# Kernel optimization log

Measured on AMD Instinct MI355X. Metric: run time of the kernel, lower is better.

The kernel has to match this reference:

```python
import jax, jax.numpy as jnp
import numpy as np

# Cost coefficients from MatcherConfig (init_kwargs)
C_CLASS, C_MASK, C_DICE, C_DIST, C_NLL, C_LIK = 2.0, 5.0, 5.0, 1.0, 0.5, 0.5

B, P, Q, E = 8, 16384, 256, 128  # images, pixels (H*W), queries, electrons


def setup_inputs() -> dict:
    key = jax.random.key(0)
    ks = jax.random.split(key, 8)
    mask_mask = jax.random.uniform(ks[0], (B, P, Q)) < 0.10           # sparsity pattern of pred logits
    mask_logit_values = jax.random.normal(ks[1], (B, P, Q), jnp.float32)
    seg_occ = jax.random.uniform(ks[2], (B, P, E)) < 0.05              # sparsity pattern of target segmap
    seg_vals = jax.random.uniform(ks[3], (B, P, E), jnp.float32, 1e-3, 1.0)
    segmap_values = jnp.where(seg_occ, seg_vals, 0.0)
    pred_logits = jax.random.normal(ks[4], (B, Q), jnp.float32)
    pred_positions = jax.random.uniform(ks[5], (B, Q, 2), jnp.float32)
    true_positions = jax.random.uniform(ks[6], (B, E, 2), jnp.float32)
    kd, ko = jax.random.split(ks[7])
    diag = 1.0 + 2.0 * jax.random.uniform(kd, (B, Q, 2), jnp.float32)  # positive diag of scale_tril
    off = 0.3 * jax.random.normal(ko, (B, Q), jnp.float32)
    pred_chol = jnp.zeros((B, Q, 2, 2), jnp.float32)
    pred_chol = pred_chol.at[..., 0, 0].set(diag[..., 0])
    pred_chol = pred_chol.at[..., 1, 1].set(diag[..., 1])
    pred_chol = pred_chol.at[..., 1, 0].set(off)
    image_sizes_xy = jnp.full((B, 2), 128.0, jnp.float32)
    return {
        'pred_logits': pred_logits,
        'mask_logit_values': mask_logit_values,
        'mask_mask': mask_mask,
        'segmap_values': segmap_values,
        'pred_positions': pred_positions,
        'pred_chol': pred_chol,
        'true_positions': true_positions,
        'image_sizes_xy': image_sizes_xy,
    }


def _total_cost(pred_logits, mask_logit_values, segmap_values, pred_positions,
                pred_chol, true_positions, image_sizes_xy, mask_mask):
    sp = jax.nn.softplus
    m = mask_mask
    # --- class cost: BCE(logit, 1) per query -> [B,Q]
    class_cost = sp(-pred_logits)
    # --- mask BCE cost (get_bce_cost): sparse entries only
    pos = jnp.where(m, sp(-mask_logit_values), 0.0)   # BCE vs 1 on nnz entries
    neg = jnp.where(m, sp(mask_logit_values), 0.0)    # BCE vs 0 on nnz entries
    targ = (segmap_values > 0).astype(pos.dtype)      # binarized target segmap
    pos_loss = jnp.einsum('bpq,bpe->bqe', pos, targ)
    neg_loss = neg.sum(1)[:, :, None] - jnp.einsum('bpq,bpe->bqe', neg, targ)
    nnz = jnp.maximum(targ.sum((1, 2)), 1.0)          # target _nnz() per image
    mask_cost = (pos_loss + neg_loss) / nnz[:, None, None]
    # --- dice cost (get_dice_cost): sparse softmax over query dim
    NEG = jnp.asarray(-1e30, mask_logit_values.dtype)
    z = jnp.where(m, mask_logit_values, NEG)
    mx = jnp.max(z, axis=-1, keepdims=True)
    ez = jnp.where(m, jnp.exp(z - mx), 0.0)
    s = ez.sum(-1, keepdims=True)
    pred_p = jnp.where(s > 0, ez / jnp.maximum(s, 1e-30), 0.0)  # [B,P,Q]
    num = 2.0 * jnp.einsum('bpq,bpe->bqe', pred_p, segmap_values)
    den = pred_p.sum(1)[:, :, None] + segmap_values.sum(1)[:, None, :]
    dice_cost = 1.0 - (num + 1.0) / (den + 1.0)
    # --- huber distance cost (delta=1), mean over xy
    d = pred_positions[:, :, None, :] - true_positions[:, None, :, :]  # [B,Q,E,2]
    ad = jnp.abs(d)
    huber_cost = jnp.where(ad < 1.0, 0.5 * d * d, ad - 0.5).mean(-1)
    # --- NLL / likelihood distance costs (MVN with scale_tril)
    mu = pred_positions * image_sizes_xy[:, None, :]
    y = true_positions * image_sizes_xy[:, None, :]
    diff = y[:, None, :, :] - mu[:, :, None, :]        # [B,Q,E,2]
    L00 = pred_chol[..., 0, 0][:, :, None]
    L10 = pred_chol[..., 1, 0][:, :, None]
    L11 = pred_chol[..., 1, 1][:, :, None]
    z0 = diff[..., 0] / L00
    z1 = (diff[..., 1] - L10 * z0) / L11
    nll_cost = 0.5 * (z0 * z0 + z1 * z1) + jnp.log(2.0 * jnp.pi) + jnp.log(L00) + jnp.log(L11)
    lik_cost = 1.0 - jnp.exp(-nll_cost)
    total = (C_CLASS * class_cost[:, :, None] + C_MASK * mask_cost + C_DICE * dice_cost
             + C_DIST * huber_cost + C_NLL * nll_cost + C_LIK * lik_cost)
    return total  # [B, Q, E] stacked per-image cost matrices


def reference(pred_logits, mask_logit_values, mask_mask, segmap_values,
              pred_positions, pred_chol, true_positions, image_sizes_xy):
    return _total_cost(pred_logits, mask_logit_values, segmap_values, pred_positions,
                       pred_chol, true_positions, image_sizes_xy, mask_mask)
```

## Files before the change

kernel.cpp:

```cpp
#include <hip/hip_runtime.h>
#include <cstdint>
#include <cstddef>

typedef float v4f __attribute__((ext_vector_type(4)));
typedef short short8 __attribute__((ext_vector_type(8)));

constexpr int B_ = 8, P_ = 16384, Q_ = 256, E_ = 128;

__device__ __forceinline__ unsigned int f2bf(float f) {
  unsigned int x = __float_as_uint(f);
  x += 0x7FFFu + ((x >> 16) & 1u);
  return x >> 16;
}
__device__ __forceinline__ float softplus_f(float x) {
  return fmaxf(x, 0.f) + __logf(1.f + __expf(-fabsf(x)));
}
__device__ __forceinline__ float wsum(float v) {
#pragma unroll
  for (int o = 32; o; o >>= 1) v += __shfl_xor(v, o, 64);
  return v;
}
__device__ __forceinline__ void lds_barrier() {
  asm volatile("s_waitcnt lgkmcnt(0)" ::: "memory");
  __builtin_amdgcn_s_barrier();
}

#define ZW 15360
__device__ __forceinline__ short8 ldfrag(const unsigned int* lds, int rowbase, int quad) {
  const int a = (quad < 2) ? (rowbase + 4 * quad) : ZW;
  union { unsigned int u[4]; short8 s; } x;
  *(uint2*)(x.u)     = *(const uint2*)(lds + a);
  *(uint2*)(x.u + 2) = *(const uint2*)(lds + a + 2);
  return x.s;
}

template<bool DIRECT>
__global__ __launch_bounds__(1024) void fused_all(
    const float* __restrict__ mlv, const int* __restrict__ mask,
    const float* __restrict__ seg, float* __restrict__ part,
    float* __restrict__ negsum, float* __restrict__ ppsum,
    float* __restrict__ segsum, float* __restrict__ nnzb)
{
  __shared__ __align__(16) unsigned int lds[15376];

  const int t = threadIdx.x, w = t >> 6, l = t & 63;
  const int lm = l & 15, quad = l >> 4;
  const int wr = w & 3, wc = w >> 2;
  const int kw = w >> 1, kh = w & 1;
  const int b = blockIdx.x >> 5, ks = blockIdx.x & 31;

  if (t < 4) lds[ZW + t] = 0u;

  v4f acc0[4][2], acc1[4][2];
#pragma unroll
  for (int i = 0; i < 4; ++i)
#pragma unroll
    for (int j = 0; j < 2; ++j) { acc0[i][j] = (v4f)0.f; acc1[i][j] = (v4f)0.f; }
  float accN[4] = {0.f,0.f,0.f,0.f};
  float accP[4] = {0.f,0.f,0.f,0.f};
  float accS[2] = {0.f,0.f};
  float cnt = 0.f;

  const float* mp = mlv + ((size_t)b * P_ + ks * 512 + w) * Q_ + l;
  const int*   kp = mask + ((size_t)b * P_ + ks * 512 + w) * Q_ + l;
  const float* sp = seg + ((size_t)b * P_ + ks * 512 + w) * E_ + l;

  float X[4]; int M[4]; float S[2];
#pragma unroll
  for (int j = 0; j < 4; ++j) { X[j] = mp[64 * j]; M[j] = kp[64 * j]; }
  S[0] = sp[0]; S[1] = sp[64];

  for (int it = 0; it < 32; ++it) {
    const int bb = (it & 1) * 7680;

    float xs[4]; int ms[4]; float sv[2];
#pragma unroll
    for (int j = 0; j < 4; ++j) { xs[j] = X[j]; ms[j] = M[j]; }
    sv[0] = S[0]; sv[1] = S[1];

    if (it < 31) {
      mp += 16 * Q_; kp += 16 * Q_; sp += 16 * E_;
#pragma unroll
      for (int j = 0; j < 4; ++j) { X[j] = mp[64 * j]; M[j] = kp[64 * j]; }
      S[0] = sp[0]; S[1] = sp[64];
    }

    float ez[4], s = 0.f;
#pragma unroll
    for (int j = 0; j < 4; ++j) {
      const float e = ms[j] ? __expf(xs[j]) : 0.f;
      ez[j] = e; s += e;
      accN[j] += __logf(1.f + e);
    }
    s = wsum(s);
    const float inv = (s > 0.f) ? (1.f / s) : 0.f;

    unsigned short* hs = (unsigned short*)lds;
#pragma unroll
    for (int j = 0; j < 4; ++j) {
      const int q = l + 64 * j;
      const float p = ez[j] * inv;
      accP[j] += p;
      hs[(bb + q * 10 + kw) * 2 + kh]        = (unsigned short)f2bf(ms[j] ? -xs[j] : 0.f);
      hs[(bb + 2560 + q * 10 + kw) * 2 + kh] = (unsigned short)f2bf(p);
    }
#pragma unroll
    for (int jj = 0; jj < 2; ++jj) {
      const int e = l + 64 * jj;
      accS[jj] += sv[jj];
      cnt += (sv[jj] > 0.f) ? 1.f : 0.f;
      hs[(bb + 5120 + e * 10 + kw) * 2 + kh] = (sv[jj] > 0.f) ? (unsigned short)0x3F80 : (unsigned short)0;
      hs[(bb + 6400 + e * 10 + kw) * 2 + kh] = (unsigned short)f2bf(sv[jj]);
    }

    lds_barrier();

#pragma unroll
    for (int j2 = 0; j2 < 2; ++j2) {
      const int eb = wc * 32 + j2 * 16 + lm;
      const short8 bf0 = ldfrag(lds, bb + 5120 + eb * 10, quad);
      const short8 bf1 = ldfrag(lds, bb + 6400 + eb * 10, quad);
#pragma unroll
      for (int i = 0; i < 4; ++i) {
        const int qa = wr * 64 + i * 16 + lm;
        const short8 af0 = ldfrag(lds, bb + qa * 10, quad);
        const short8 af1 = ldfrag(lds, bb + 2560 + qa * 10, quad);
        acc0[i][j2] = __builtin_amdgcn_mfma_f32_16x16x32_bf16(af0, bf0, acc0[i][j2], 0, 0, 0);
        acc1[i][j2] = __builtin_amdgcn_mfma_f32_16x16x32_bf16(af1, bf1, acc1[i][j2], 0, 0, 0);
      }
    }
  }

  __syncthreads();
  float* fr = (float*)lds;
#pragma unroll
  for (int j = 0; j < 4; ++j) {
    fr[w * 256 + l + 64 * j] = accN[j];
    fr[4096 + w * 256 + l + 64 * j] = accP[j];
  }
#pragma unroll
  for (int jj = 0; jj < 2; ++jj)
    fr[8192 + w * 128 + l + 64 * jj] = accS[jj];
  __syncthreads();
  if (t < 256) {
    float sn = 0.f, sq = 0.f;
#pragma unroll
    for (int k = 0; k < 16; ++k) { sn += fr[k * 256 + t]; sq += fr[4096 + k * 256 + t]; }
    atomicAdd(&negsum[b * 256 + t], sn);
    atomicAdd(&ppsum[b * 256 + t], sq);
  } else if (t < 384) {
    const int e = t - 256;
    float ss = 0.f;
#pragma unroll
    for (int k = 0; k < 16; ++k) ss += fr[8192 + k * 128 + e];
    atomicAdd(&segsum[b * 128 + e], ss);
  }
  cnt = wsum(cnt);
  if (l == 0) atomicAdd(&nnzb[b], cnt);

  if constexpr (DIRECT) {
    float* p0 = part + ((size_t)(ks * 8 + b) * 2) * 32768;
    float* p1 = p0 + 32768;
#pragma unroll
    for (int i = 0; i < 4; ++i)
#pragma unroll
      for (int r = 0; r < 4; ++r) {
        const int q = wr * 64 + i * 16 + quad * 4 + r;
#pragma unroll
        for (int j2 = 0; j2 < 2; ++j2) {
          const int e = wc * 32 + j2 * 16 + lm;
          p0[q * 128 + e] = acc0[i][j2][r];
          p1[q * 128 + e] = acc1[i][j2][r];
        }
      }
  } else {
    float* p0 = part + (size_t)b * 32768;
    float* p1 = part + (size_t)(8 + b) * 32768;
#pragma unroll
    for (int i = 0; i < 4; ++i)
#pragma unroll
      for (int r = 0; r < 4; ++r) {
        const int q = wr * 64 + i * 16 + quad * 4 + r;
#pragma unroll
        for (int j2 = 0; j2 < 2; ++j2) {
          const int e = wc * 32 + j2 * 16 + lm;
          atomicAdd(&p0[q * 128 + e], acc0[i][j2][r]);
          atomicAdd(&p1[q * 128 + e], acc1[i][j2][r]);
        }
      }
  }
}

template<bool DIRECT>
__global__ __launch_bounds__(128) void epilogue(
    const float* __restrict__ part,
    const float* __restrict__ negsum, const float* __restrict__ ppsum,
    const float* __restrict__ segsum, const float* __restrict__ nnzb,
    const float* __restrict__ logits, const float* __restrict__ ppos,
    const float* __restrict__ chol, const float* __restrict__ tpos,
    const float* __restrict__ imgsz, float* __restrict__ out)
{
  const int bq = blockIdx.x;
  const int b = bq >> 8;
  const int e = threadIdx.x;
  const int qe = (bq & 255) * 128 + e;

  float g1, g2;
  if constexpr (DIRECT) {
    g1 = 0.f; g2 = 0.f;
#pragma unroll 8
    for (int ksi = 0; ksi < 32; ++ksi) {
      g1 += part[((size_t)(ksi * 8 + b) * 2) * 32768 + qe];
      g2 += part[((size_t)(ksi * 8 + b) * 2 + 1) * 32768 + qe];
    }
  } else {
    g1 = part[(size_t)b * 32768 + qe];
    g2 = part[(size_t)(8 + b) * 32768 + qe];
  }

  const float nnz = fmaxf(nnzb[b], 1.f);
  const float mask_cost = (negsum[bq] + g1) / nnz;
  const float dice = 1.f - (2.f * g2 + 1.f) / (ppsum[bq] + segsum[b * 128 + e] + 1.f);
  const float cls = softplus_f(-logits[bq]);
  const float px = ppos[bq * 2], py = ppos[bq * 2 + 1];
  const float tx = tpos[(b * 128 + e) * 2], ty = tpos[(b * 128 + e) * 2 + 1];
  const float dx = px - tx, dy = py - ty;
  const float ax = fabsf(dx), ay = fabsf(dy);
  const float hx = (ax < 1.f) ? 0.5f * dx * dx : ax - 0.5f;
  const float hy = (ay < 1.f) ? 0.5f * dy * dy : ay - 0.5f;
  const float huber = 0.5f * (hx + hy);
  const float sx = imgsz[b * 2], sy = imgsz[b * 2 + 1];
  const float L00 = chol[bq * 4 + 0], L10 = chol[bq * 4 + 2], L11 = chol[bq * 4 + 3];
  const float d0 = (tx - px) * sx, d1 = (ty - py) * sy;
  const float z0 = d0 / L00;
  const float z1 = (d1 - L10 * z0) / L11;
  const float nll = 0.5f * (z0 * z0 + z1 * z1) + 1.8378770664093453f + __logf(L00) + __logf(L11);
  const float lik = 1.f - __expf(-nll);
  out[bq * 128 + e] = 2.f * cls + 5.f * mask_cost + 5.f * dice + huber + 0.5f * nll + 0.5f * lik;
}

extern "C" void kernel_launch(void* const* d_in, const int* in_sizes, int n_in,
                              void* d_out, int out_size, void* d_ws, size_t ws_size,
                              hipStream_t stream)
{
  (void)in_sizes; (void)n_in; (void)out_size;
  const float* logits = (const float*)d_in[0];
  const float* mlv    = (const float*)d_in[1];
  const int*   mask   = (const int*)d_in[2];
  const float* seg    = (const float*)d_in[3];
  const float* ppos   = (const float*)d_in[4];
  const float* chol   = (const float*)d_in[5];
  const float* tpos   = (const float*)d_in[6];
  const float* imgsz  = (const float*)d_in[7];

  char* ws = (char*)d_ws;
  const size_t PART_DIRECT = 67108864ull;
  const size_t NEED = PART_DIRECT + 20512ull;

  if (ws_size >= NEED) {
    float* part   = (float*)ws;
    float* negsum = (float*)(ws + PART_DIRECT);
    float* ppsum  = (float*)(ws + PART_DIRECT + 8192);
    float* segsum = (float*)(ws + PART_DIRECT + 16384);
    float* nnzb   = (float*)(ws + PART_DIRECT + 20480);
    hipMemsetAsync(ws + PART_DIRECT, 0, 20512, stream);
    fused_all<true><<<256, 1024, 0, stream>>>(mlv, mask, seg, part, negsum, ppsum, segsum, nnzb);
    epilogue<true><<<2048, 128, 0, stream>>>(part, negsum, ppsum, segsum, nnzb,
                                             logits, ppos, chol, tpos, imgsz, (float*)d_out);
  } else {
    float* part   = (float*)(ws);
    float* negsum = (float*)(ws + 2097152);
    float* ppsum  = (float*)(ws + 2105344);
    float* segsum = (float*)(ws + 2113536);
    float* nnzb   = (float*)(ws + 2117632);
    hipMemsetAsync(ws, 0, 2117664, stream);
    fused_all<false><<<256, 1024, 0, stream>>>(mlv, mask, seg, part, negsum, ppsum, segsum, nnzb);
    epilogue<false><<<2048, 128, 0, stream>>>(part, negsum, ppsum, segsum, nnzb,
                                              logits, ppos, chol, tpos, imgsz, (float*)d_out);
  }
}
```

Measured before the change: 457.0 us.

## Split expert dimension across blocks and repack LDS tiles as swizzled bf16 pairs

The fused kernel now launches 512 blocks of 512 threads, where each block covers half of the E columns. Each wave processes two pixels per step and writes packed 32-bit bf16 pairs into a single XOR-swizzled LDS buffer, so fragments can be read with 128-bit loads instead of scattered 16-bit stores and 64-bit reads. The aim is to cut LDS store and bank-conflict overhead and to raise occupancy with smaller blocks. In exchange, the mask logits, mask and exp/log work on the Q side are now read and computed twice, once per E half, and a second barrier replaces the double buffering.

```diff
diff --git a/kernel.cpp b/kernel.cpp
--- a/kernel.cpp
+++ b/kernel.cpp
@@ -25,31 +25,28 @@
   __builtin_amdgcn_s_barrier();
 }
 
-#define ZW 15360
-__device__ __forceinline__ short8 ldfrag(const unsigned int* lds, int rowbase, int quad) {
-  const int a = (quad < 2) ? (rowbase + 4 * quad) : ZW;
-  union { unsigned int u[4]; short8 s; } x;
-  *(uint2*)(x.u)     = *(const uint2*)(lds + a);
-  *(uint2*)(x.u + 2) = *(const uint2*)(lds + a + 2);
-  return x.s;
-}
-
 template<bool DIRECT>
-__global__ __launch_bounds__(1024) void fused_all(
+__global__ __launch_bounds__(512, 4) void fused_all(
     const float* __restrict__ mlv, const int* __restrict__ mask,
     const float* __restrict__ seg, float* __restrict__ part,
     float* __restrict__ negsum, float* __restrict__ ppsum,
     float* __restrict__ segsum, float* __restrict__ nnzb)
 {
-  __shared__ __align__(16) unsigned int lds[15376];
+  __shared__ __align__(16) unsigned int lds[5120];
+  unsigned int* A1 = lds;
+  unsigned int* EZ = lds + 2048;
+  unsigned int* SB = lds + 4096;
+  unsigned int* ST = lds + 4608;
 
   const int t = threadIdx.x, w = t >> 6, l = t & 63;
   const int lm = l & 15, quad = l >> 4;
   const int wr = w & 3, wc = w >> 2;
-  const int kw = w >> 1, kh = w & 1;
-  const int b = blockIdx.x >> 5, ks = blockIdx.x & 31;
-
-  if (t < 4) lds[ZW + t] = 0u;
+  const int eh = blockIdx.x >> 8;
+  const int b  = (blockIdx.x >> 5) & 7;
+  const int ks = blockIdx.x & 31;
+  const int wx   = w ^ ((l & 1) << 2);
+  const int qsel = 4 * (quad ^ (lm & 1));
+  const bool hasd = (quad < 2);
 
   v4f acc0[4][2], acc1[4][2];
 #pragma unroll
@@ -58,75 +55,85 @@
     for (int j = 0; j < 2; ++j) { acc0[i][j] = (v4f)0.f; acc1[i][j] = (v4f)0.f; }
   float accN[4] = {0.f,0.f,0.f,0.f};
   float accP[4] = {0.f,0.f,0.f,0.f};
-  float accS[2] = {0.f,0.f};
-  float cnt = 0.f;
-
-  const float* mp = mlv + ((size_t)b * P_ + ks * 512 + w) * Q_ + l;
-  const int*   kp = mask + ((size_t)b * P_ + ks * 512 + w) * Q_ + l;
-  const float* sp = seg + ((size_t)b * P_ + ks * 512 + w) * E_ + l;
-
-  float X[4]; int M[4]; float S[2];
-#pragma unroll
-  for (int j = 0; j < 4; ++j) { X[j] = mp[64 * j]; M[j] = kp[64 * j]; }
-  S[0] = sp[0]; S[1] = sp[64];
+  float accS = 0.f, cnt = 0.f;
+
+  const float* mp = mlv + ((size_t)b * P_ + ks * 512 + 2 * w) * Q_ + l;
+  const int*   kp = mask + ((size_t)b * P_ + ks * 512 + 2 * w) * Q_ + l;
+  const float* sp = seg + ((size_t)b * P_ + ks * 512 + 2 * w) * E_ + eh * 64 + l;
+
+  float X0[4], X1[4]; int M0[4], M1[4]; float S0, S1;
+#pragma unroll
+  for (int j = 0; j < 4; ++j) {
+    X0[j] = mp[64 * j]; X1[j] = mp[Q_ + 64 * j];
+    M0[j] = kp[64 * j]; M1[j] = kp[Q_ + 64 * j];
+  }
+  S0 = sp[0]; S1 = sp[E_];
 
   for (int it = 0; it < 32; ++it) {
-    const int bb = (it & 1) * 7680;
-
-    float xs[4]; int ms[4]; float sv[2];
-#pragma unroll
-    for (int j = 0; j < 4; ++j) { xs[j] = X[j]; ms[j] = M[j]; }
-    sv[0] = S[0]; sv[1] = S[1];
+    float ez0[4], ez1[4]; unsigned a1w[4];
+    float s0 = 0.f, s1 = 0.f;
+#pragma unroll
+    for (int j = 0; j < 4; ++j) {
+      const bool m0 = M0[j] != 0, m1 = M1[j] != 0;
+      a1w[j] = f2bf(m0 ? -X0[j] : 0.f) | (f2bf(m1 ? -X1[j] : 0.f) << 16);
+      const float e0 = m0 ? __expf(X0[j]) : 0.f;
+      const float e1 = m1 ? __expf(X1[j]) : 0.f;
+      ez0[j] = e0; ez1[j] = e1; s0 += e0; s1 += e1;
+      accN[j] += __logf(1.f + e0) + __logf(1.f + e1);
+    }
+    const unsigned sbw = ((S0 > 0.f) ? 0x3F80u : 0u) | ((S1 > 0.f) ? 0x3F800000u : 0u);
+    const unsigned stw = f2bf(S0) | (f2bf(S1) << 16);
+    accS += S0 + S1;
+    cnt  += ((S0 > 0.f) ? 1.f : 0.f) + ((S1 > 0.f) ? 1.f : 0.f);
 
     if (it < 31) {
       mp += 16 * Q_; kp += 16 * Q_; sp += 16 * E_;
 #pragma unroll
-      for (int j = 0; j < 4; ++j) { X[j] = mp[64 * j]; M[j] = kp[64 * j]; }
-      S[0] = sp[0]; S[1] = sp[64];
-    }
-
-    float ez[4], s = 0.f;
+      for (int j = 0; j < 4; ++j) {
+        X0[j] = mp[64 * j]; X1[j] = mp[Q_ + 64 * j];
+        M0[j] = kp[64 * j]; M1[j] = kp[Q_ + 64 * j];
+      }
+      S0 = sp[0]; S1 = sp[E_];
+    }
+
+    s0 = wsum(s0); s1 = wsum(s1);
+    const float i0 = (s0 > 0.f) ? (1.f / s0) : 0.f;
+    const float i1 = (s1 > 0.f) ? (1.f / s1) : 0.f;
+    unsigned ezw[4];
 #pragma unroll
     for (int j = 0; j < 4; ++j) {
-      const float e = ms[j] ? __expf(xs[j]) : 0.f;
-      ez[j] = e; s += e;
-      accN[j] += __logf(1.f + e);
-    }
-    s = wsum(s);
-    const float inv = (s > 0.f) ? (1.f / s) : 0.f;
-
-    unsigned short* hs = (unsigned short*)lds;
+      const float p0 = ez0[j] * i0, p1 = ez1[j] * i1;
+      accP[j] += p0 + p1;
+      ezw[j] = f2bf(p0) | (f2bf(p1) << 16);
+    }
+
+    lds_barrier();
 #pragma unroll
     for (int j = 0; j < 4; ++j) {
-      const int q = l + 64 * j;
-      const float p = ez[j] * inv;
-      accP[j] += p;
-      hs[(bb + q * 10 + kw) * 2 + kh]        = (unsigned short)f2bf(ms[j] ? -xs[j] : 0.f);
-      hs[(bb + 2560 + q * 10 + kw) * 2 + kh] = (unsigned short)f2bf(p);
-    }
-#pragma unroll
-    for (int jj = 0; jj < 2; ++jj) {
-      const int e = l + 64 * jj;
-      accS[jj] += sv[jj];
-      cnt += (sv[jj] > 0.f) ? 1.f : 0.f;
-      hs[(bb + 5120 + e * 10 + kw) * 2 + kh] = (sv[jj] > 0.f) ? (unsigned short)0x3F80 : (unsigned short)0;
-      hs[(bb + 6400 + e * 10 + kw) * 2 + kh] = (unsigned short)f2bf(sv[jj]);
-    }
-
+      A1[8 * l + 512 * j + wx] = a1w[j];
+      EZ[8 * l + 512 * j + wx] = ezw[j];
+    }
+    SB[8 * l + wx] = sbw;
+    ST[8 * l + wx] = stw;
     lds_barrier();
 
+    const short8 z8 = {0,0,0,0,0,0,0,0};
+    short8 af0[4], af1[4];
+#pragma unroll
+    for (int i = 0; i < 4; ++i) {
+      const int a = (wr * 64 + i * 16 + lm) * 8 + qsel;
+      af0[i] = hasd ? *(const short8*)(A1 + a) : z8;
+      af1[i] = hasd ? *(const short8*)(EZ + a) : z8;
+    }
 #pragma unroll
     for (int j2 = 0; j2 < 2; ++j2) {
-      const int eb = wc * 32 + j2 * 16 + lm;
-      const short8 bf0 = ldfrag(lds, bb + 5120 + eb * 10, quad);
-      const short8 bf1 = ldfrag(lds, bb + 6400 + eb * 10, quad);
+      const int bb = (wc * 32 + j2 * 16 + lm) * 8 + qsel;
+      const short8 bf0 = hasd ? *(const short8*)(SB + bb) : z8;
+      const short8 bf1 = hasd ? *(const short8*)(ST + bb) : z8;
 #pragma unroll
       for (int i = 0; i < 4; ++i) {
-        const int qa = wr * 64 + i * 16 + lm;
-        const short8 af0 = ldfrag(lds, bb + qa * 10, quad);
-        const short8 af1 = ldfrag(lds, bb + 2560 + qa * 10, quad);
-        acc0[i][j2] = __builtin_amdgcn_mfma_f32_16x16x32_bf16(af0, bf0, acc0[i][j2], 0, 0, 0);
-        acc1[i][j2] = __builtin_amdgcn_mfma_f32_16x16x32_bf16(af1, bf1, acc1[i][j2], 0, 0, 0);
+        acc0[i][j2] = __builtin_amdgcn_mfma_f32_16x16x32_bf16(af0[i], bf0, acc0[i][j2], 0, 0, 0);
+        acc1[i][j2] = __builtin_amdgcn_mfma_f32_16x16x32_bf16(af1[i], bf1, acc1[i][j2], 0, 0, 0);
       }
     }
   }
@@ -136,24 +143,24 @@
 #pragma unroll
   for (int j = 0; j < 4; ++j) {
     fr[w * 256 + l + 64 * j] = accN[j];
-    fr[4096 + w * 256 + l + 64 * j] = accP[j];
-  }
-#pragma unroll
-  for (int jj = 0; jj < 2; ++jj)
-    fr[8192 + w * 128 + l + 64 * jj] = accS[jj];
+    fr[2048 + w * 256 + l + 64 * j] = accP[j];
+  }
+  fr[4096 + w * 64 + l] = accS;
   __syncthreads();
   if (t < 256) {
     float sn = 0.f, sq = 0.f;
 #pragma unroll
-    for (int k = 0; k < 16; ++k) { sn += fr[k * 256 + t]; sq += fr[4096 + k * 256 + t]; }
-    atomicAdd(&negsum[b * 256 + t], sn);
-    atomicAdd(&ppsum[b * 256 + t], sq);
-  } else if (t < 384) {
+    for (int k = 0; k < 8; ++k) { sn += fr[k * 256 + t]; sq += fr[2048 + k * 256 + t]; }
+    if (eh == 0) {
+      atomicAdd(&negsum[b * 256 + t], sn);
+      atomicAdd(&ppsum[b * 256 + t], sq);
+    }
+  } else if (t < 320) {
     const int e = t - 256;
     float ss = 0.f;
 #pragma unroll
-    for (int k = 0; k < 16; ++k) ss += fr[8192 + k * 128 + e];
-    atomicAdd(&segsum[b * 128 + e], ss);
+    for (int k = 0; k < 8; ++k) ss += fr[4096 + k * 64 + e];
+    atomicAdd(&segsum[b * 128 + eh * 64 + e], ss);
   }
   cnt = wsum(cnt);
   if (l == 0) atomicAdd(&nnzb[b], cnt);
@@ -168,9 +175,9 @@
         const int q = wr * 64 + i * 16 + quad * 4 + r;
 #pragma unroll
         for (int j2 = 0; j2 < 2; ++j2) {
-          const int e = wc * 32 + j2 * 16 + lm;
-          p0[q * 128 + e] = acc0[i][j2][r];
-          p1[q * 128 + e] = acc1[i][j2][r];
+          const int eg = eh * 64 + wc * 32 + j2 * 16 + lm;
+          p0[q * 128 + eg] = acc0[i][j2][r];
+          p1[q * 128 + eg] = acc1[i][j2][r];
         }
       }
   } else {
@@ -183,9 +190,9 @@
         const int q = wr * 64 + i * 16 + quad * 4 + r;
 #pragma unroll
         for (int j2 = 0; j2 < 2; ++j2) {
-          const int e = wc * 32 + j2 * 16 + lm;
-          atomicAdd(&p0[q * 128 + e], acc0[i][j2][r]);
-          atomicAdd(&p1[q * 128 + e], acc1[i][j2][r]);
+          const int eg = eh * 64 + wc * 32 + j2 * 16 + lm;
+          atomicAdd(&p0[q * 128 + eg], acc0[i][j2][r]);
+          atomicAdd(&p1[q * 128 + eg], acc1[i][j2][r]);
         }
       }
   }
@@ -264,7 +271,7 @@
     float* segsum = (float*)(ws + PART_DIRECT + 16384);
     float* nnzb   = (float*)(ws + PART_DIRECT + 20480);
     hipMemsetAsync(ws + PART_DIRECT, 0, 20512, stream);
-    fused_all<true><<<256, 1024, 0, stream>>>(mlv, mask, seg, part, negsum, ppsum, segsum, nnzb);
+    fused_all<true><<<512, 512, 0, stream>>>(mlv, mask, seg, part, negsum, ppsum, segsum, nnzb);
     epilogue<true><<<2048, 128, 0, stream>>>(part, negsum, ppsum, segsum, nnzb,
                                              logits, ppos, chol, tpos, imgsz, (float*)d_out);
   } else {
@@ -274,7 +281,7 @@
     float* segsum = (float*)(ws + 2113536);
     float* nnzb   = (float*)(ws + 2117632);
     hipMemsetAsync(ws, 0, 2117664, stream);
-    fused_all<false><<<256, 1024, 0, stream>>>(mlv, mask, seg, part, negsum, ppsum, segsum, nnzb);
+    fused_all<false><<<512, 512, 0, stream>>>(mlv, mask, seg, part, negsum, ppsum, segsum, nnzb);
     epilogue<false><<<2048, 128, 0, stream>>>(part, negsum, ppsum, segsum, nnzb,
                                               logits, ppos, chol, tpos, imgsz, (float*)d_out);
   }
```

Result: slower. 952.4 us (+108.4%).
